# Kernel tuning notes

Measured on AMD Instinct MI355X. Metric: run time of the kernel, lower is better.

The kernel has to match this reference:

```python
import math
import jax, jax.numpy as jnp
import numpy as np

B, L, D = 2, 2048, 512
S, P = 4, 16  # n_orthogonal_sets, planes_per_set
TP = S * P


def setup_inputs() -> dict:
    key = jax.random.key(0)
    ks = jax.random.split(key, 12)
    sc = 0.02
    return {
        "x": jax.random.normal(ks[0], (B, L, D), dtype=jnp.float32),
        "set_weights": jnp.ones((S,), dtype=jnp.float32),
        "kw1": jax.random.normal(ks[1], (D, D), dtype=jnp.float32) * sc,
        "kb1": jnp.zeros((D,), dtype=jnp.float32),
        "kw2": jax.random.normal(ks[2], (D, TP), dtype=jnp.float32) * sc,
        "kb2": jnp.zeros((TP,), dtype=jnp.float32),
        "qw1": jax.random.normal(ks[3], (D, D), dtype=jnp.float32) * sc,
        "qb1": jnp.zeros((D,), dtype=jnp.float32),
        "qw2": jax.random.normal(ks[4], (D, TP), dtype=jnp.float32) * sc,
        "qb2": jnp.zeros((TP,), dtype=jnp.float32),
        "vw": jax.random.normal(ks[5], (D, D), dtype=jnp.float32) * sc,
        "vb": jnp.zeros((D,), dtype=jnp.float32),
        "ln_g": jnp.ones((D,), dtype=jnp.float32),
        "ln_b": jnp.zeros((D,), dtype=jnp.float32),
        "ow": jax.random.normal(ks[6], (D, D), dtype=jnp.float32) * sc,
        "ob": jnp.zeros((D,), dtype=jnp.float32),
    }


def reference(x, set_weights, kw1, kb1, kw2, kb2, qw1, qb1, qw2, qb2, vw, vb, ln_g, ln_b, ow, ob):
    b, l, d = x.shape
    # phase encoders: Linear -> GELU(exact) -> Linear, tanh * pi
    kp = jnp.tanh(jax.nn.gelu(x @ kw1 + kb1, approximate=False) @ kw2 + kb2) * math.pi
    qp = jnp.tanh(jax.nn.gelu(x @ qw1 + qb1, approximate=False) @ qw2 + qb2) * math.pi
    kp = kp.reshape(b, l, S, P)
    qp = qp.reshape(b, l, S, P)
    V = x @ vw + vb  # real values; phasor complex handled as (re, im)
    w = jax.nn.softmax(set_weights)
    total = jnp.zeros((b, l, d), dtype=x.dtype)
    for s in range(S):
        kc, ksn = jnp.cos(kp[:, :, s, :]), jnp.sin(kp[:, :, s, :])  # [b,l,P]
        # bound = e^{i kp} * V (V real); memory = cumsum over time
        Mre = jnp.cumsum(kc[..., None] * V[:, :, None, :], axis=1)  # [b,l,P,d]
        Mim = jnp.cumsum(ksn[..., None] * V[:, :, None, :], axis=1)
        # Re(memory * conj(e^{i qp})) summed over planes
        r = (jnp.einsum('blpd,blp->bld', Mre, jnp.cos(qp[:, :, s, :]))
             + jnp.einsum('blpd,blp->bld', Mim, jnp.sin(qp[:, :, s, :])))
        total = total + w[s] * r
    positions = jnp.arange(1, l + 1, dtype=x.dtype)
    norm = jnp.sqrt(positions * P)[None, :, None]
    y = total / norm
    mu = jnp.mean(y, axis=-1, keepdims=True)
    var = jnp.mean((y - mu) ** 2, axis=-1, keepdims=True)
    yn = (y - mu) / jnp.sqrt(var + 1e-5) * ln_g + ln_b
    return x + yn @ ow + ob
```

## Files before the change

kernel.cpp:

```cpp
#include <hip/hip_runtime.h>
#include <math.h>

constexpr int NB = 2;
constexpr int LQ = 2048;
constexpr int DD = 512;
constexpr int PPL = 16;
constexpr int TPP = 64;
constexpr int FF = 128;
constexpr int NC = 32;
constexpr int TC = 64;
constexpr float PI_F = 3.14159265358979323846f;

typedef __attribute__((ext_vector_type(4))) float f32x4;
typedef __attribute__((ext_vector_type(8))) short bf16x8;

static __device__ __forceinline__ unsigned short f2bf(float x) {
    union { float f; unsigned u; } v; v.f = x;
    unsigned r = v.u + 0x7fff + ((v.u >> 16) & 1);
    return (unsigned short)(r >> 16);
}
static __device__ __forceinline__ float bf2f(unsigned short u) {
    union { unsigned u; float f; } v; v.u = ((unsigned)u) << 16;
    return v.f;
}

__global__ __launch_bounds__(256) void prep_kernel(
    const float* __restrict__ kw1, const float* __restrict__ qw1,
    const float* __restrict__ vw, const float* __restrict__ ow,
    const float* __restrict__ kw2, const float* __restrict__ qw2,
    unsigned short* __restrict__ kw1t, unsigned short* __restrict__ qw1t,
    unsigned short* __restrict__ vwt, unsigned short* __restrict__ owt,
    unsigned short* __restrict__ kw2t, unsigned short* __restrict__ qw2t)
{
    __shared__ float t[32][33];
    const int id = blockIdx.x;
    const int tid = threadIdx.x;
    const float* W;
    unsigned short* O;
    int K, N, n0, k0;
    if (id < 1024) {
        const int mat = id >> 8, rem = id & 255;
        W = (mat == 0) ? kw1 : (mat == 1) ? qw1 : (mat == 2) ? vw : ow;
        O = (mat == 0) ? kw1t : (mat == 1) ? qw1t : (mat == 2) ? vwt : owt;
        K = DD; N = DD;
        n0 = (rem & 15) * 32; k0 = (rem >> 4) * 32;
    } else {
        const int rid = id - 1024;
        const int mat = rid >> 5, rem = rid & 31;
        W = mat ? qw2 : kw2;
        O = mat ? qw2t : kw2t;
        K = DD; N = TPP;
        n0 = (rem & 1) * 32; k0 = (rem >> 1) * 32;
    }
    const int tx = tid & 31, ty = tid >> 5;
#pragma unroll
    for (int i = 0; i < 4; ++i)
        t[ty + 8 * i][tx] = W[(size_t)(k0 + ty + 8 * i) * N + n0 + tx];
    __syncthreads();
#pragma unroll
    for (int i = 0; i < 4; ++i)
        O[(size_t)(n0 + ty + 8 * i) * K + k0 + tx] = f2bf(t[tx][ty + 8 * i]);
}

__global__ __launch_bounds__(256) void mgemm_fused(
    const float* __restrict__ X,
    const unsigned short* __restrict__ kw1t, const unsigned short* __restrict__ qw1t,
    const unsigned short* __restrict__ vwt,
    const float* __restrict__ kb1, const float* __restrict__ qb1, const float* __restrict__ vb,
    unsigned short* __restrict__ hkb, unsigned short* __restrict__ hqb,
    unsigned short* __restrict__ Vt)
{
    const int z = blockIdx.z;
    const unsigned short* Bt = (z == 0) ? kw1t : (z == 1) ? qw1t : vwt;
    const float* bias = (z == 0) ? kb1 : (z == 1) ? qb1 : vb;
    unsigned short* obf = (z == 0) ? hkb : (z == 1) ? hqb : Vt;
    const int K = DD, N = DD;

    __shared__ unsigned short As[128 * 72];
    __shared__ unsigned short Bs[128 * 72];
    const int tid = threadIdx.x;
    const int w = tid >> 6, lane = tid & 63, grp = lane >> 4, lid = lane & 15;
    const int wr = w >> 1, wc = w & 1;
    const int row0 = blockIdx.y * 128, col0 = blockIdx.x * 128;
    f32x4 acc[4][4];
#pragma unroll
    for (int m = 0; m < 4; ++m)
#pragma unroll
        for (int n = 0; n < 4; ++n) acc[m][n] = (f32x4)0.f;

    for (int k0 = 0; k0 < K; k0 += 64) {
        float4 a0[4], a1[4];
        bf16x8 vbv[4];
#pragma unroll
        for (int i = 0; i < 4; ++i) {
            const int c = tid + i * 256;
            const float* ap = X + (size_t)(row0 + (c >> 3)) * K + k0 + (c & 7) * 8;
            a0[i] = *(const float4*)ap;
            a1[i] = *(const float4*)(ap + 4);
            vbv[i] = *(const bf16x8*)(Bt + (size_t)(col0 + (c >> 3)) * K + k0 + (c & 7) * 8);
        }
        __syncthreads();
#pragma unroll
        for (int i = 0; i < 4; ++i) {
            const int c = tid + i * 256;
            ushort4 u0 = {f2bf(a0[i].x), f2bf(a0[i].y), f2bf(a0[i].z), f2bf(a0[i].w)};
            ushort4 u1 = {f2bf(a1[i].x), f2bf(a1[i].y), f2bf(a1[i].z), f2bf(a1[i].w)};
            *(ushort4*)(As + (c >> 3) * 72 + (c & 7) * 8) = u0;
            *(ushort4*)(As + (c >> 3) * 72 + (c & 7) * 8 + 4) = u1;
            *(bf16x8*)(Bs + (c >> 3) * 72 + (c & 7) * 8) = vbv[i];
        }
        __syncthreads();
#pragma unroll
        for (int kk = 0; kk < 2; ++kk) {
            bf16x8 af[4], bfr[4];
#pragma unroll
            for (int m = 0; m < 4; ++m)
                af[m] = *(const bf16x8*)(As + (wr * 64 + m * 16 + lid) * 72 + kk * 32 + grp * 8);
#pragma unroll
            for (int n = 0; n < 4; ++n)
                bfr[n] = *(const bf16x8*)(Bs + (wc * 64 + n * 16 + lid) * 72 + kk * 32 + grp * 8);
#pragma unroll
            for (int m = 0; m < 4; ++m)
#pragma unroll
                for (int n = 0; n < 4; ++n)
                    acc[m][n] = __builtin_amdgcn_mfma_f32_16x16x32_bf16(af[m], bfr[n], acc[m][n], 0, 0, 0);
        }
    }
#pragma unroll
    for (int m = 0; m < 4; ++m) {
#pragma unroll
        for (int n = 0; n < 4; ++n) {
            const int col = col0 + wc * 64 + n * 16 + lid;
            const float bc = bias[col];
            if (z == 2) {
                const int rowb = row0 + wr * 64 + m * 16 + grp * 4;
                const int b = rowb >> 11, l = rowb & (LQ - 1);
                const int c = l >> 6, t0 = l & 63;
                ushort4 u;
                u.x = f2bf(acc[m][n][0] + bc);
                u.y = f2bf(acc[m][n][1] + bc);
                u.z = f2bf(acc[m][n][2] + bc);
                u.w = f2bf(acc[m][n][3] + bc);
                *(ushort4*)(Vt + ((size_t)((b * NC + c) * DD) + col) * TC + t0) = u;
            } else {
#pragma unroll
                for (int r = 0; r < 4; ++r) {
                    const int row = row0 + wr * 64 + m * 16 + grp * 4 + r;
                    float v = acc[m][n][r] + bc;
                    v = 0.5f * v * (1.0f + erff(v * 0.70710678118654752f));
                    obf[(size_t)row * N + col] = f2bf(v);
                }
            }
        }
    }
}

__global__ __launch_bounds__(256) void phase_fused(
    const unsigned short* __restrict__ hkb, const unsigned short* __restrict__ hqb,
    const unsigned short* __restrict__ kw2t, const unsigned short* __restrict__ qw2t,
    const float* __restrict__ kb2, const float* __restrict__ qb2,
    const float* __restrict__ sw,
    unsigned short* __restrict__ CKb, unsigned short* __restrict__ CQb,
    unsigned short* __restrict__ CKt)
{
    const int isq = blockIdx.y;
    const unsigned short* A = isq ? hqb : hkb;
    const unsigned short* Bt = isq ? qw2t : kw2t;
    const float* b2 = isq ? qb2 : kb2;
    unsigned short* FROW = isq ? CQb : CKb;
    const int K = DD;

    __shared__ unsigned short As[64 * 72];
    __shared__ unsigned short Bs[64 * 72];
    const int tid = threadIdx.x;
    const int w = tid >> 6, lane = tid & 63, grp = lane >> 4, lid = lane & 15;
    const int row0 = blockIdx.x * 64;
    f32x4 acc[4];
#pragma unroll
    for (int n = 0; n < 4; ++n) acc[n] = (f32x4)0.f;

    for (int k0 = 0; k0 < K; k0 += 64) {
        bf16x8 va[2], vbv[2];
#pragma unroll
        for (int i = 0; i < 2; ++i) {
            const int c = tid + i * 256;
            va[i] = *(const bf16x8*)(A + (size_t)(row0 + (c >> 3)) * K + k0 + (c & 7) * 8);
            vbv[i] = *(const bf16x8*)(Bt + (size_t)(c >> 3) * K + k0 + (c & 7) * 8);
        }
        __syncthreads();
#pragma unroll
        for (int i = 0; i < 2; ++i) {
            const int c = tid + i * 256;
            *(bf16x8*)(As + (c >> 3) * 72 + (c & 7) * 8) = va[i];
            *(bf16x8*)(Bs + (c >> 3) * 72 + (c & 7) * 8) = vbv[i];
        }
        __syncthreads();
#pragma unroll
        for (int kk = 0; kk < 2; ++kk) {
            bf16x8 af, bfr[4];
            af = *(const bf16x8*)(As + (w * 16 + lid) * 72 + kk * 32 + grp * 8);
#pragma unroll
            for (int n = 0; n < 4; ++n)
                bfr[n] = *(const bf16x8*)(Bs + (n * 16 + lid) * 72 + kk * 32 + grp * 8);
#pragma unroll
            for (int n = 0; n < 4; ++n)
                acc[n] = __builtin_amdgcn_mfma_f32_16x16x32_bf16(af, bfr[n], acc[n], 0, 0, 0);
        }
    }
    float wsm[4] = {1.f, 1.f, 1.f, 1.f};
    if (isq) {
        float s0 = sw[0], s1 = sw[1], s2 = sw[2], s3 = sw[3];
        float mx = fmaxf(fmaxf(s0, s1), fmaxf(s2, s3));
        float e0 = __expf(s0 - mx), e1 = __expf(s1 - mx), e2 = __expf(s2 - mx), e3 = __expf(s3 - mx);
        float inv = 1.0f / (e0 + e1 + e2 + e3);
        wsm[0] = e0 * inv; wsm[1] = e1 * inv; wsm[2] = e2 * inv; wsm[3] = e3 * inv;
    }
#pragma unroll
    for (int n = 0; n < 4; ++n) {
        const int p = n * 16 + lid;
        const float bc = b2[p];
        const float wg = isq ? wsm[p >> 4] : 1.0f;
#pragma unroll
        for (int r = 0; r < 4; ++r) {
            const int row = row0 + w * 16 + grp * 4 + r;
            float u = acc[n][r] + bc;
            float th = 1.0f - 2.0f / (__expf(2.0f * u) + 1.0f);
            float ph = th * PI_F;
            float sp, cp;
            __sincosf(ph, &sp, &cp);
            const unsigned short cb = f2bf(cp * wg), sb = f2bf(sp * wg);
            FROW[(size_t)row * FF + 2 * p + 0] = cb;
            FROW[(size_t)row * FF + 2 * p + 1] = sb;
            if (!isq) {
                const int b = row >> 11, l = row & (LQ - 1);
                const int c = l >> 6, t = l & 63;
                const size_t base = ((size_t)(b * NC + c) * FF) * TC;
                CKt[base + (size_t)(2 * p + 0) * TC + t] = cb;
                CKt[base + (size_t)(2 * p + 1) * TC + t] = sb;
            }
        }
    }
}

__global__ __launch_bounds__(256) void passA_mfma(
    const unsigned short* __restrict__ Vt, const unsigned short* __restrict__ CKt,
    unsigned short* __restrict__ Stp)
{
    const int tid = threadIdx.x;
    const int w = tid >> 6, lane = tid & 63, grp = lane >> 4, lid = lane & 15;
    const int dq = blockIdx.x, c = blockIdx.y, b = blockIdx.z;
    const int d0 = dq * 128 + w * 32;
    const size_t cb = (size_t)(b * NC + c);
    f32x4 acc[2][8];
#pragma unroll
    for (int md = 0; md < 2; ++md)
#pragma unroll
        for (int nf = 0; nf < 8; ++nf) acc[md][nf] = (f32x4)0.f;
#pragma unroll
    for (int kt = 0; kt < 2; ++kt) {
        bf16x8 av[2], bk[8];
#pragma unroll
        for (int md = 0; md < 2; ++md)
            av[md] = *(const bf16x8*)(Vt + (cb * DD + d0 + md * 16 + lid) * TC + kt * 32 + grp * 8);
#pragma unroll
        for (int nf = 0; nf < 8; ++nf)
            bk[nf] = *(const bf16x8*)(CKt + (cb * FF + nf * 16 + lid) * TC + kt * 32 + grp * 8);
#pragma unroll
        for (int md = 0; md < 2; ++md)
#pragma unroll
            for (int nf = 0; nf < 8; ++nf)
                acc[md][nf] = __builtin_amdgcn_mfma_f32_16x16x32_bf16(av[md], bk[nf], acc[md][nf], 0, 0, 0);
    }
#pragma unroll
    for (int md = 0; md < 2; ++md)
#pragma unroll
        for (int nf = 0; nf < 8; ++nf)
#pragma unroll
            for (int r = 0; r < 4; ++r) {
                const int d = d0 + md * 16 + grp * 4 + r;
                const int f = nf * 16 + lid;
                Stp[(cb * DD + d) * FF + f] = f2bf(acc[md][nf][r]);
            }
}

__global__ __launch_bounds__(256) void prefix_mfma(
    const unsigned short* __restrict__ Stp, unsigned short* __restrict__ Stb)
{
    const int gid = blockIdx.x * 256 + threadIdx.x;
    const int b = gid >> 16;
    const int df = gid & 65535;
    float run = 0.f;
#pragma unroll
    for (int c = 0; c < NC; ++c) {
        const size_t idx = ((size_t)(b * NC + c) << 16) + df;
        Stb[idx] = f2bf(run);
        run += bf2f(Stp[idx]);
    }
}

__global__ __launch_bounds__(256) void passC_mfma(
    const unsigned short* __restrict__ CQb, const unsigned short* __restrict__ CKb,
    const unsigned short* __restrict__ Vt, const unsigned short* __restrict__ Stb,
    float* __restrict__ R)
{
    __shared__ unsigned short P[64][72];
    const int tid = threadIdx.x;
    const int w = tid >> 6, lane = tid & 63, grp = lane >> 4, lid = lane & 15;
    const int dh = blockIdx.x, c = blockIdx.y, b = blockIdx.z;
    const size_t rowbase = (size_t)b * LQ + c * 64;
    const size_t cb = (size_t)(b * NC + c);
    f32x4 qk[4];
#pragma unroll
    for (int nt = 0; nt < 4; ++nt) qk[nt] = (f32x4)0.f;
#pragma unroll
    for (int kf = 0; kf < 4; ++kf) {
        bf16x8 aq = *(const bf16x8*)(CQb + (rowbase + w * 16 + lid) * FF + kf * 32 + grp * 8);
        bf16x8 bk[4];
#pragma unroll
        for (int nt = 0; nt < 4; ++nt)
            bk[nt] = *(const bf16x8*)(CKb + (rowbase + nt * 16 + lid) * FF + kf * 32 + grp * 8);
#pragma unroll
        for (int nt = 0; nt < 4; ++nt)
            qk[nt] = __builtin_amdgcn_mfma_f32_16x16x32_bf16(aq, bk[nt], qk[nt], 0, 0, 0);
    }
#pragma unroll
    for (int nt = 0; nt < 4; ++nt)
#pragma unroll
        for (int r = 0; r < 4; ++r) {
            const int row = w * 16 + grp * 4 + r;
            const int col = nt * 16 + lid;
            P[row][col] = f2bf(col <= row ? qk[nt][r] : 0.f);
        }
    __syncthreads();
    const int d0 = dh * 128 + w * 32;
    f32x4 racc[4][2];
#pragma unroll
    for (int ml = 0; ml < 4; ++ml)
#pragma unroll
        for (int nd = 0; nd < 2; ++nd) racc[ml][nd] = (f32x4)0.f;
#pragma unroll
    for (int kt = 0; kt < 2; ++kt) {
        bf16x8 ap[4], bv[2];
#pragma unroll
        for (int ml = 0; ml < 4; ++ml)
            ap[ml] = *(const bf16x8*)&P[ml * 16 + lid][kt * 32 + grp * 8];
#pragma unroll
        for (int nd = 0; nd < 2; ++nd)
            bv[nd] = *(const bf16x8*)(Vt + (cb * DD + d0 + nd * 16 + lid) * TC + kt * 32 + grp * 8);
#pragma unroll
        for (int ml = 0; ml < 4; ++ml)
#pragma unroll
            for (int nd = 0; nd < 2; ++nd)
                racc[ml][nd] = __builtin_amdgcn_mfma_f32_16x16x32_bf16(ap[ml], bv[nd], racc[ml][nd], 0, 0, 0);
    }
#pragma unroll
    for (int kf = 0; kf < 4; ++kf) {
        bf16x8 aq[4], bs[2];
#pragma unroll
        for (int ml = 0; ml < 4; ++ml)
            aq[ml] = *(const bf16x8*)(CQb + (rowbase + ml * 16 + lid) * FF + kf * 32 + grp * 8);
#pragma unroll
        for (int nd = 0; nd < 2; ++nd)
            bs[nd] = *(const bf16x8*)(Stb + (cb * DD + d0 + nd * 16 + lid) * FF + kf * 32 + grp * 8);
#pragma unroll
        for (int ml = 0; ml < 4; ++ml)
#pragma unroll
            for (int nd = 0; nd < 2; ++nd)
                racc[ml][nd] = __builtin_amdgcn_mfma_f32_16x16x32_bf16(aq[ml], bs[nd], racc[ml][nd], 0, 0, 0);
    }
#pragma unroll
    for (int ml = 0; ml < 4; ++ml)
#pragma unroll
        for (int nd = 0; nd < 2; ++nd)
#pragma unroll
            for (int r = 0; r < 4; ++r) {
                const int l = ml * 16 + grp * 4 + r;
                const int d = d0 + nd * 16 + lid;
                R[(rowbase + l) * DD + d] = racc[ml][nd][r];
            }
}

__global__ __launch_bounds__(256) void ln_kernel(
    const float* __restrict__ R, const float* __restrict__ g,
    const float* __restrict__ be, unsigned short* __restrict__ YN)
{
    const int row = blockIdx.x;
    const int l = row & (LQ - 1);
    const int tid = threadIdx.x;
    const float pscale = rsqrtf((float)((l + 1) * PPL));
    float y0 = R[(size_t)row * DD + tid] * pscale;
    float y1 = R[(size_t)row * DD + 256 + tid] * pscale;
    float s = y0 + y1;
    float q = y0 * y0 + y1 * y1;
#pragma unroll
    for (int off = 32; off >= 1; off >>= 1) {
        s += __shfl_xor(s, off, 64);
        q += __shfl_xor(q, off, 64);
    }
    __shared__ float rs[4], rq[4];
    const int wid = tid >> 6, lane = tid & 63;
    if (lane == 0) { rs[wid] = s; rq[wid] = q; }
    __syncthreads();
    const float ts = rs[0] + rs[1] + rs[2] + rs[3];
    const float tq = rq[0] + rq[1] + rq[2] + rq[3];
    const float mu = ts * (1.0f / DD);
    float var = tq * (1.0f / DD) - mu * mu;
    const float rstd = rsqrtf(var + 1e-5f);
    YN[(size_t)row * DD + tid] = f2bf((y0 - mu) * rstd * g[tid] + be[tid]);
    YN[(size_t)row * DD + 256 + tid] = f2bf((y1 - mu) * rstd * g[tid + 256] + be[tid + 256]);
}

__global__ __launch_bounds__(256) void mgemm_out(
    const unsigned short* __restrict__ A, const unsigned short* __restrict__ Bt,
    const float* __restrict__ bias, const float* __restrict__ resid,
    float* __restrict__ out)
{
    const int K = DD, N = DD;
    __shared__ unsigned short As[128 * 72];
    __shared__ unsigned short Bs[64 * 72];
    const int tid = threadIdx.x;
    const int w = tid >> 6, lane = tid & 63, grp = lane >> 4, lid = lane & 15;
    const int wr = w >> 1, wc = w & 1;
    const int row0 = blockIdx.y * 128, col0 = blockIdx.x * 64;
    f32x4 acc[4][2];
#pragma unroll
    for (int m = 0; m < 4; ++m)
#pragma unroll
        for (int n = 0; n < 2; ++n) acc[m][n] = (f32x4)0.f;

    for (int k0 = 0; k0 < K; k0 += 64) {
        bf16x8 va[4], vbv[2];
#pragma unroll
        for (int i = 0; i < 4; ++i) {
            const int c = tid + i * 256;
            va[i] = *(const bf16x8*)(A + (size_t)(row0 + (c >> 3)) * K + k0 + (c & 7) * 8);
        }
#pragma unroll
        for (int i = 0; i < 2; ++i) {
            const int c = tid + i * 256;
            vbv[i] = *(const bf16x8*)(Bt + (size_t)(col0 + (c >> 3)) * K + k0 + (c & 7) * 8);
        }
        __syncthreads();
#pragma unroll
        for (int i = 0; i < 4; ++i) {
            const int c = tid + i * 256;
            *(bf16x8*)(As + (c >> 3) * 72 + (c & 7) * 8) = va[i];
        }
#pragma unroll
        for (int i = 0; i < 2; ++i) {
            const int c = tid + i * 256;
            *(bf16x8*)(Bs + (c >> 3) * 72 + (c & 7) * 8) = vbv[i];
        }
        __syncthreads();
#pragma unroll
        for (int kk = 0; kk < 2; ++kk) {
            bf16x8 af[4], bfr[2];
#pragma unroll
            for (int m = 0; m < 4; ++m)
                af[m] = *(const bf16x8*)(As + (wr * 64 + m * 16 + lid) * 72 + kk * 32 + grp * 8);
#pragma unroll
            for (int n = 0; n < 2; ++n)
                bfr[n] = *(const bf16x8*)(Bs + (wc * 32 + n * 16 + lid) * 72 + kk * 32 + grp * 8);
#pragma unroll
            for (int m = 0; m < 4; ++m)
#pragma unroll
                for (int n = 0; n < 2; ++n)
                    acc[m][n] = __builtin_amdgcn_mfma_f32_16x16x32_bf16(af[m], bfr[n], acc[m][n], 0, 0, 0);
        }
    }
#pragma unroll
    for (int m = 0; m < 4; ++m) {
#pragma unroll
        for (int n = 0; n < 2; ++n) {
            const int col = col0 + wc * 32 + n * 16 + lid;
            const float bc = bias[col];
#pragma unroll
            for (int r = 0; r < 4; ++r) {
                const int row = row0 + wr * 64 + m * 16 + grp * 4 + r;
                out[(size_t)row * N + col] = acc[m][n][r] + bc + resid[(size_t)row * N + col];
            }
        }
    }
}

extern "C" void kernel_launch(void* const* d_in, const int* in_sizes, int n_in,
                              void* d_out, int out_size, void* d_ws, size_t ws_size,
                              hipStream_t stream)
{
    const float* x   = (const float*)d_in[0];
    const float* sw  = (const float*)d_in[1];
    const float* kw1 = (const float*)d_in[2];
    const float* kb1 = (const float*)d_in[3];
    const float* kw2 = (const float*)d_in[4];
    const float* kb2 = (const float*)d_in[5];
    const float* qw1 = (const float*)d_in[6];
    const float* qb1 = (const float*)d_in[7];
    const float* qw2 = (const float*)d_in[8];
    const float* qb2 = (const float*)d_in[9];
    const float* vw  = (const float*)d_in[10];
    const float* vb  = (const float*)d_in[11];
    const float* lng = (const float*)d_in[12];
    const float* lnb = (const float*)d_in[13];
    const float* ow  = (const float*)d_in[14];
    const float* ob  = (const float*)d_in[15];
    float* out = (float*)d_out;

    const size_t MR = (size_t)NB * LQ;
    float* ws = (float*)d_ws;
    float* Rb = ws;
    unsigned short* hkb  = (unsigned short*)(Rb + MR * DD);
    unsigned short* hqb  = hkb + MR * DD;
    unsigned short* YNb  = hqb + MR * DD;
    unsigned short* Vt   = YNb + MR * DD;
    unsigned short* CQb  = Vt + MR * DD;
    unsigned short* CKb  = CQb + MR * FF;
    unsigned short* CKt  = CKb + MR * FF;
    unsigned short* Stp  = CKt + MR * FF;
    unsigned short* Stb  = Stp + (size_t)NB * NC * DD * FF;
    unsigned short* kw1t = Stb + (size_t)NB * NC * DD * FF;
    unsigned short* qw1t = kw1t + (size_t)DD * DD;
    unsigned short* vwt  = qw1t + (size_t)DD * DD;
    unsigned short* owt  = vwt + (size_t)DD * DD;
    unsigned short* kw2t = owt + (size_t)DD * DD;
    unsigned short* qw2t = kw2t + (size_t)TPP * DD;

    const dim3 blk(256);
    hipLaunchKernelGGL(prep_kernel, dim3(1088), blk, 0, stream,
                       kw1, qw1, vw, ow, kw2, qw2,
                       kw1t, qw1t, vwt, owt, kw2t, qw2t);
    hipLaunchKernelGGL(mgemm_fused, dim3(DD / 128, MR / 128, 3), blk, 0, stream,
                       x, kw1t, qw1t, vwt, kb1, qb1, vb, hkb, hqb, Vt);
    hipLaunchKernelGGL(phase_fused, dim3(MR / 64, 2), blk, 0, stream,
                       hkb, hqb, kw2t, qw2t, kb2, qb2, sw, CKb, CQb, CKt);
    hipLaunchKernelGGL(passA_mfma, dim3(4, NC, NB), blk, 0, stream, Vt, CKt, Stp);
    hipLaunchKernelGGL(prefix_mfma, dim3((NB * DD * FF) / 256), blk, 0, stream, Stp, Stb);
    hipLaunchKernelGGL(passC_mfma, dim3(4, NC, NB), blk, 0, stream, CQb, CKb, Vt, Stb, Rb);
    hipLaunchKernelGGL(ln_kernel, dim3((unsigned)MR), blk, 0, stream, Rb, lng, lnb, YNb);
    hipLaunchKernelGGL(mgemm_out, dim3(DD / 64, MR / 128), blk, 0, stream, YNb, owt, ob, x, out);
}
```

Baseline: 157.5 us.

## Pre-convert x to bf16 and use direct global-to-LDS loads with XOR swizzle

Adds a pass in the prep kernel that converts x to bf16 once, so the fused input GEMM no longer reads fp32 x and converts it per tile for each of its three weight matrices. The GEMM's tile loading now uses global_load_lds 16-byte direct-to-LDS transfers into an unpadded, XOR-swizzled shared layout instead of going through registers. This lowers global traffic and register staging, at the cost of an extra bf16 buffer write and read and one more workspace region.

Result: no change. 154.9 us (-1.7%).

```diff
diff --git a/kernel.cpp b/kernel.cpp
--- a/kernel.cpp
+++ b/kernel.cpp
@@ -24,10 +24,16 @@
     return v.f;
 }
 
+#define GLOAD16(gp, lp) __builtin_amdgcn_global_load_lds( \
+    (const __attribute__((address_space(1))) unsigned int*)(gp), \
+    (__attribute__((address_space(3))) unsigned int*)(lp), 16, 0, 0)
+
 __global__ __launch_bounds__(256) void prep_kernel(
+    const float* __restrict__ x,
     const float* __restrict__ kw1, const float* __restrict__ qw1,
     const float* __restrict__ vw, const float* __restrict__ ow,
     const float* __restrict__ kw2, const float* __restrict__ qw2,
+    unsigned short* __restrict__ xb,
     unsigned short* __restrict__ kw1t, unsigned short* __restrict__ qw1t,
     unsigned short* __restrict__ vwt, unsigned short* __restrict__ owt,
     unsigned short* __restrict__ kw2t, unsigned short* __restrict__ qw2t)
@@ -35,17 +41,28 @@
     __shared__ float t[32][33];
     const int id = blockIdx.x;
     const int tid = threadIdx.x;
+    if (id < 1024) {
+        const int i = id * 2048 + tid * 8;
+        float4 a = *(const float4*)(x + i);
+        float4 b = *(const float4*)(x + i + 4);
+        ushort4 u0 = {f2bf(a.x), f2bf(a.y), f2bf(a.z), f2bf(a.w)};
+        ushort4 u1 = {f2bf(b.x), f2bf(b.y), f2bf(b.z), f2bf(b.w)};
+        *(ushort4*)(xb + i) = u0;
+        *(ushort4*)(xb + i + 4) = u1;
+        return;
+    }
     const float* W;
     unsigned short* O;
     int K, N, n0, k0;
-    if (id < 1024) {
-        const int mat = id >> 8, rem = id & 255;
+    if (id < 2048) {
+        const int rid = id - 1024;
+        const int mat = rid >> 8, rem = rid & 255;
         W = (mat == 0) ? kw1 : (mat == 1) ? qw1 : (mat == 2) ? vw : ow;
         O = (mat == 0) ? kw1t : (mat == 1) ? qw1t : (mat == 2) ? vwt : owt;
         K = DD; N = DD;
         n0 = (rem & 15) * 32; k0 = (rem >> 4) * 32;
     } else {
-        const int rid = id - 1024;
+        const int rid = id - 2048;
         const int mat = rid >> 5, rem = rid & 31;
         W = mat ? qw2 : kw2;
         O = mat ? qw2t : kw2t;
@@ -63,7 +80,7 @@
 }
 
 __global__ __launch_bounds__(256) void mgemm_fused(
-    const float* __restrict__ X,
+    const unsigned short* __restrict__ A,
     const unsigned short* __restrict__ kw1t, const unsigned short* __restrict__ qw1t,
     const unsigned short* __restrict__ vwt,
     const float* __restrict__ kb1, const float* __restrict__ qb1, const float* __restrict__ vb,
@@ -76,12 +93,14 @@
     unsigned short* obf = (z == 0) ? hkb : (z == 1) ? hqb : Vt;
     const int K = DD, N = DD;
 
-    __shared__ unsigned short As[128 * 72];
-    __shared__ unsigned short Bs[128 * 72];
+    __shared__ unsigned short As[128 * 64];
+    __shared__ unsigned short Bs[128 * 64];
     const int tid = threadIdx.x;
     const int w = tid >> 6, lane = tid & 63, grp = lane >> 4, lid = lane & 15;
     const int wr = w >> 1, wc = w & 1;
     const int row0 = blockIdx.y * 128, col0 = blockIdx.x * 128;
+    const int l8 = lane >> 3, s8 = lane & 7;
+    const int q = s8 ^ l8;
     f32x4 acc[4][4];
 #pragma unroll
     for (int m = 0; m < 4; ++m)
@@ -89,36 +108,25 @@
         for (int n = 0; n < 4; ++n) acc[m][n] = (f32x4)0.f;
 
     for (int k0 = 0; k0 < K; k0 += 64) {
-        float4 a0[4], a1[4];
-        bf16x8 vbv[4];
-#pragma unroll
-        for (int i = 0; i < 4; ++i) {
-            const int c = tid + i * 256;
-            const float* ap = X + (size_t)(row0 + (c >> 3)) * K + k0 + (c & 7) * 8;
-            a0[i] = *(const float4*)ap;
-            a1[i] = *(const float4*)(ap + 4);
-            vbv[i] = *(const bf16x8*)(Bt + (size_t)(col0 + (c >> 3)) * K + k0 + (c & 7) * 8);
-        }
         __syncthreads();
 #pragma unroll
-        for (int i = 0; i < 4; ++i) {
-            const int c = tid + i * 256;
-            ushort4 u0 = {f2bf(a0[i].x), f2bf(a0[i].y), f2bf(a0[i].z), f2bf(a0[i].w)};
-            ushort4 u1 = {f2bf(a1[i].x), f2bf(a1[i].y), f2bf(a1[i].z), f2bf(a1[i].w)};
-            *(ushort4*)(As + (c >> 3) * 72 + (c & 7) * 8) = u0;
-            *(ushort4*)(As + (c >> 3) * 72 + (c & 7) * 8 + 4) = u1;
-            *(bf16x8*)(Bs + (c >> 3) * 72 + (c & 7) * 8) = vbv[i];
+        for (int j = 0; j < 4; ++j) {
+            const int rbase = w * 32 + j * 8;
+            const int lrow = rbase + l8;
+            GLOAD16(A  + (size_t)(row0 + lrow) * K + k0 + q * 8, As + rbase * 64);
+            GLOAD16(Bt + (size_t)(col0 + lrow) * K + k0 + q * 8, Bs + rbase * 64);
         }
         __syncthreads();
 #pragma unroll
         for (int kk = 0; kk < 2; ++kk) {
+            const int xr = lid & 7;
             bf16x8 af[4], bfr[4];
 #pragma unroll
             for (int m = 0; m < 4; ++m)
-                af[m] = *(const bf16x8*)(As + (wr * 64 + m * 16 + lid) * 72 + kk * 32 + grp * 8);
+                af[m] = *(const bf16x8*)(As + (wr * 64 + m * 16 + lid) * 64 + (((kk * 4 + grp) ^ xr) * 8));
 #pragma unroll
             for (int n = 0; n < 4; ++n)
-                bfr[n] = *(const bf16x8*)(Bs + (wc * 64 + n * 16 + lid) * 72 + kk * 32 + grp * 8);
+                bfr[n] = *(const bf16x8*)(Bs + (wc * 64 + n * 16 + lid) * 64 + (((kk * 4 + grp) ^ xr) * 8));
 #pragma unroll
             for (int m = 0; m < 4; ++m)
 #pragma unroll
@@ -508,7 +516,8 @@
     const size_t MR = (size_t)NB * LQ;
     float* ws = (float*)d_ws;
     float* Rb = ws;
-    unsigned short* hkb  = (unsigned short*)(Rb + MR * DD);
+    unsigned short* xb   = (unsigned short*)(Rb + MR * DD);
+    unsigned short* hkb  = xb + MR * DD;
     unsigned short* hqb  = hkb + MR * DD;
     unsigned short* YNb  = hqb + MR * DD;
     unsigned short* Vt   = YNb + MR * DD;
@@ -525,11 +534,11 @@
     unsigned short* qw2t = kw2t + (size_t)TPP * DD;
 
     const dim3 blk(256);
-    hipLaunchKernelGGL(prep_kernel, dim3(1088), blk, 0, stream,
-                       kw1, qw1, vw, ow, kw2, qw2,
-                       kw1t, qw1t, vwt, owt, kw2t, qw2t);
+    hipLaunchKernelGGL(prep_kernel, dim3(2112), blk, 0, stream,
+                       x, kw1, qw1, vw, ow, kw2, qw2,
+                       xb, kw1t, qw1t, vwt, owt, kw2t, qw2t);
     hipLaunchKernelGGL(mgemm_fused, dim3(DD / 128, MR / 128, 3), blk, 0, stream,
-                       x, kw1t, qw1t, vwt, kb1, qb1, vb, hkb, hqb, Vt);
+                       xb, kw1t, qw1t, vwt, kb1, qb1, vb, hkb, hqb, Vt);
     hipLaunchKernelGGL(phase_fused, dim3(MR / 64, 2), blk, 0, stream,
                        hkb, hqb, kw2t, qw2t, kb2, qb2, sw, CKb, CQb, CKt);
     hipLaunchKernelGGL(passA_mfma, dim3(4, NC, NB), blk, 0, stream, Vt, CKt, Stp);
```
